# Optimization experiments

Measured on AMD Instinct MI355X. Metric: run time of the kernel, lower is better.

## Reference

```python
import jax, jax.numpy as jnp
import numpy as np

B, T, DMODEL = 2, 2048, 1024
H, DK, DV = 16, 64, 64
FF = 4096
EPS = 1e-5


def _layernorm_2d(x):
    # torch LayerNorm(normalized_shape=(T, dmodel)): normalize jointly over last two
    # dims, biased variance, weight=1 / bias=0 (freshly constructed each forward).
    mu = jnp.mean(x, axis=(1, 2), keepdims=True)
    var = jnp.mean((x - mu) ** 2, axis=(1, 2), keepdims=True)
    return (x - mu) / jnp.sqrt(var + EPS)


def setup_inputs() -> dict:
    key = jax.random.key(0)
    ks = jax.random.split(key, 9)
    s = 0.02  # small init for numerical sanity (original uses uniform(-1,1))
    return {
        "x": jax.random.normal(ks[0], (B, T, DMODEL), jnp.float32),
        "Wq": jax.random.normal(ks[1], (H, DMODEL, DK), jnp.float32) * s,
        "Wk": jax.random.normal(ks[2], (H, DMODEL, DK), jnp.float32) * s,
        "Wv": jax.random.normal(ks[3], (H, DMODEL, DV), jnp.float32) * s,
        "Wo": jax.random.normal(ks[4], (DMODEL, DMODEL), jnp.float32) * s,
        "W1": jax.random.normal(ks[5], (DMODEL, FF), jnp.float32) * s,
        "b1": jnp.zeros((FF,), jnp.float32),
        "W2": jax.random.normal(ks[6], (FF, DMODEL), jnp.float32) * s,
        "b2": jnp.zeros((DMODEL,), jnp.float32),
    }


def reference(x, Wq, Wk, Wv, Wo, W1, b1, W2, b2):
    b, t, d = x.shape
    h, _, dk = Wq.shape
    dv = Wv.shape[-1]
    # per-head projections: (B,H,T,dk/dv)
    Qp = jnp.einsum("btd,hdk->bhtk", x, Wq)
    Kp = jnp.einsum("btd,hdk->bhtk", x, Wk)
    Vp = jnp.einsum("btd,hdv->bhtv", x, Wv)
    scores = jnp.einsum("bhqk,bhsk->bhqs", Qp, Kp) / np.sqrt(dk).astype(np.float32)
    # NOTE: original does torch.softmax(heads, 2) -> softmax over the QUERY axis
    attn = jax.nn.softmax(scores, axis=2)
    heads = jnp.einsum("bhqs,bhsv->bqhv", attn, Vp).reshape(b, t, h * dv)
    att_out = heads @ Wo
    o1 = _layernorm_2d(x + att_out)
    ff = jnp.maximum(o1 @ W1 + b1, 0.0) @ W2 + b2
    return _layernorm_2d(o1 + ff)
```

## Files before the change

### kernel.cpp

```cpp
#include <hip/hip_runtime.h>
#include <hip/hip_bf16.h>
#include <cstddef>
#include <cstdint>

typedef __hip_bfloat16 hbf;
typedef __attribute__((ext_vector_type(8))) __bf16 bf16x8;
typedef __attribute__((ext_vector_type(4))) float f32x4;

#define B_ 2
#define T_ 2048
#define D_ 1024
#define H_ 16
#define FF_ 4096
#define EPS_ 1e-5f
#define SCALE_ 0.18033688011112f

__device__ __forceinline__ float bf2f(hbf v) { return __bfloat162float(v); }
__device__ __forceinline__ float fexp2(float x) {
  return __builtin_amdgcn_exp2f(x);
}
__device__ __forceinline__ float flog2(float x) {
  return __builtin_amdgcn_logf(x);
}
__device__ __forceinline__ float ldin(const void* p, size_t i, int isbf) {
  return isbf ? __bfloat162float(((const hbf*)p)[i]) : ((const float*)p)[i];
}
__device__ __forceinline__ void ston(void* p, size_t i, float v, int isbf) {
  if (isbf) ((hbf*)p)[i] = __float2bfloat16(v);
  else ((float*)p)[i] = v;
}
__device__ __forceinline__ f32x4 mfma16(bf16x8 a, bf16x8 b, f32x4 c) {
  return __builtin_amdgcn_mfma_f32_16x16x32_bf16(a, b, c, 0, 0, 0);
}
__device__ __forceinline__ bf16x8 ldfrag(const hbf* p) {
  return *(const bf16x8*)p;
}
__device__ __forceinline__ void glds16(const hbf* g, hbf* l) {
  __builtin_amdgcn_global_load_lds(
      (const __attribute__((address_space(1))) void*)g,
      (__attribute__((address_space(3))) void*)l, 16, 0, 0);
}

__global__ __launch_bounds__(256) void detect_dtype(const unsigned* x,
                                                    int* flag) {
  __shared__ int cnt[256];
  int c = 0;
  for (int i = threadIdx.x; i < 4096; i += 256) {
    unsigned low = x[i] & 0xFFFFu;
    unsigned e = (low >> 7) & 0xFFu;
    if (e >= 100u && e <= 142u) c++;
  }
  cnt[threadIdx.x] = c;
  __syncthreads();
  for (int off = 128; off > 0; off >>= 1) {
    if ((int)threadIdx.x < off) cnt[threadIdx.x] += cnt[threadIdx.x + off];
    __syncthreads();
  }
  if (threadIdx.x == 0) *flag = (cnt[0] > 2458) ? 1 : 0;
}

__device__ __forceinline__ void tr_tile(const void* __restrict__ src,
                                        hbf* __restrict__ dst, int R, int C,
                                        size_t zoff, int cx, int ry, int f,
                                        float (*tile)[33]) {
  const int tx = threadIdx.x & 31, ty = threadIdx.x >> 5;
  const int c0 = cx * 32, r0 = ry * 32;
#pragma unroll
  for (int p = 0; p < 4; p++) {
    int rr = p * 8 + ty;
    tile[rr][tx] = ldin(src, zoff + (size_t)(r0 + rr) * C + c0 + tx, f);
  }
  __syncthreads();
#pragma unroll
  for (int p = 0; p < 4; p++) {
    int cc = p * 8 + ty;
    dst[zoff + (size_t)(c0 + cc) * R + r0 + tx] = __float2bfloat16(tile[tx][cc]);
  }
}

__global__ __launch_bounds__(256) void preconv(
    const void* __restrict__ x, const void* __restrict__ Wq,
    const void* __restrict__ Wk, const void* __restrict__ Wv,
    const void* __restrict__ Wo, const void* __restrict__ W1,
    const void* __restrict__ W2, const void* __restrict__ b1,
    const void* __restrict__ b2, hbf* __restrict__ xb,
    hbf* __restrict__ wqkvt, hbf* __restrict__ wot, hbf* __restrict__ w1t,
    hbf* __restrict__ w2t, hbf* __restrict__ b1b, hbf* __restrict__ b2b,
    const int* __restrict__ flag) {
  __shared__ float tile[32][33];
  const int f = *flag;
  const int bid = blockIdx.x;
  if (bid < 3072) {
    int which = bid >> 10;
    int r = bid & 1023;
    int z = r >> 6, rem = r & 63;
    int ry = rem >> 1, cx = rem & 1;
    const void* src = (which == 0) ? Wq : (which == 1) ? Wk : Wv;
    hbf* dst = wqkvt + (size_t)which * (D_ * D_);
    tr_tile(src, dst, 1024, 64, (size_t)z * 65536, cx, ry, f, tile);
  } else if (bid < 4096) {
    int t = bid - 3072;
    tr_tile(Wo, wot, 1024, 1024, 0, t & 31, t >> 5, f, tile);
  } else if (bid < 8192) {
    int t = bid - 4096;
    tr_tile(W1, w1t, 1024, 4096, 0, t & 127, t >> 7, f, tile);
  } else if (bid < 12288) {
    int t = bid - 8192;
    tr_tile(W2, w2t, 4096, 1024, 0, t & 31, t >> 5, f, tile);
  } else if (bid < 13312) {
    size_t base = (size_t)(bid - 12288) * 4096;
    for (int i = threadIdx.x; i < 4096; i += 256)
      xb[base + i] = __float2bfloat16(ldin(x, base + i, f));
  } else if (bid == 13312) {
    for (int i = threadIdx.x; i < FF_; i += 256)
      b1b[i] = __float2bfloat16(ldin(b1, i, f));
  } else {
    for (int i = threadIdx.x; i < D_; i += 256)
      b2b[i] = __float2bfloat16(ldin(b2, i, f));
  }
}

template <int MODE, int BM, int BN>
__global__ __launch_bounds__(256) void gemm_bt(
    const hbf* __restrict__ A, const hbf* __restrict__ Bt, hbf* __restrict__ C,
    float* __restrict__ Cf0, float* __restrict__ Cf1,
    const hbf* __restrict__ e1, float* __restrict__ red, int M, int N, int K,
    int LDK) {
  constexpr int WM = BM / 2, WN = BN / 2;
  constexpr int IF = WM / 16, JF = WN / 16;
  __shared__ alignas(16) hbf As[BM * 64];
  __shared__ alignas(16) hbf Bs[BN * 64];
  const int tid = threadIdx.x;
  const int wave = tid >> 6, lane = tid & 63;
  const int quad = lane >> 4, l16 = lane & 15;
  const int m0 = blockIdx.y * BM, n0 = blockIdx.x * BN;
  const int mw = (wave >> 1) * WM, nw = (wave & 1) * WN;
  const int srow = tid >> 3;
  const int scol = (tid & 7) * 8;
  const int kbase = (MODE == 4) ? blockIdx.z * K : 0;
  const f32x4 zero = {0.f, 0.f, 0.f, 0.f};
  f32x4 acc[IF][JF];
#pragma unroll
  for (int i = 0; i < IF; i++)
#pragma unroll
    for (int j = 0; j < JF; j++) acc[i][j] = zero;

  const hbf* ga = &A[(size_t)(m0 + srow) * LDK + kbase + scol];
  const hbf* gb = &Bt[(size_t)(n0 + srow) * LDK + kbase + scol];
  hbf* lA = &As[wave * 512];
  hbf* lB = &Bs[wave * 512];

  for (int k0 = 0; k0 < K; k0 += 64) {
#pragma unroll
    for (int c = 0; c < BM / 32; c++)
      glds16(ga + (size_t)(c * 32) * LDK + k0, lA + c * 2048);
#pragma unroll
    for (int c = 0; c < BN / 32; c++)
      glds16(gb + (size_t)(c * 32) * LDK + k0, lB + c * 2048);
    __syncthreads();
    bf16x8 af[2][IF], bfr[2][JF];
#pragma unroll
    for (int h = 0; h < 2; h++) {
#pragma unroll
      for (int i = 0; i < IF; i++)
        af[h][i] = ldfrag(&As[(mw + i * 16 + l16) * 64 + h * 32 + quad * 8]);
#pragma unroll
      for (int j = 0; j < JF; j++)
        bfr[h][j] = ldfrag(&Bs[(nw + j * 16 + l16) * 64 + h * 32 + quad * 8]);
    }
#pragma unroll
    for (int h = 0; h < 2; h++)
#pragma unroll
      for (int i = 0; i < IF; i++)
#pragma unroll
        for (int j = 0; j < JF; j++)
          acc[i][j] = mfma16(af[h][i], bfr[h][j], acc[i][j]);
    __syncthreads();
  }
  float ssum = 0.f, ssq = 0.f;
#pragma unroll
  for (int i = 0; i < IF; i++)
#pragma unroll
    for (int j = 0; j < JF; j++)
#pragma unroll
      for (int r = 0; r < 4; r++) {
        int m = m0 + mw + i * 16 + quad * 4 + r;
        int n = n0 + nw + j * 16 + l16;
        float v = acc[i][j][r];
        if (MODE == 0) {
          int which = n >> 10, n1 = n & 1023;
          int h = n1 >> 6, cc = n1 & 63;
          int b = m >> 11, t = m & (T_ - 1);
          if (which == 0) v *= SCALE_;
          C[(size_t)which * ((size_t)B_ * H_ * T_ * 64) +
            (((size_t)(b * H_ + h)) * T_ + t) * 64 + cc] = __float2bfloat16(v);
        } else if (MODE == 1) {
          hbf hv = __float2bfloat16(v + bf2f(e1[(size_t)m * N + n]));
          C[(size_t)m * N + n] = hv;
          float fv = bf2f(hv);
          ssum += fv;
          ssq += fv * fv;
        } else if (MODE == 2) {
          C[(size_t)m * N + n] = __float2bfloat16(fmaxf(v + bf2f(e1[n]), 0.f));
        } else if (MODE == 4) {
          float* Cf = blockIdx.z ? Cf1 : Cf0;
          Cf[(size_t)m * N + n] = v;
        }
      }
  if (MODE == 1) {
    float* sc = (float*)As;
    sc[tid] = ssum;
    sc[256 + tid] = ssq;
    __syncthreads();
    for (int off = 128; off > 0; off >>= 1) {
      if (tid < off) {
        sc[tid] += sc[tid + off];
        sc[256 + tid] += sc[256 + tid + off];
      }
      __syncthreads();
    }
    if (tid == 0) {
      int b = m0 >> 11;
      atomicAdd(&red[b * 2 + 0], sc[0]);
      atomicAdd(&red[b * 2 + 1], sc[256]);
    }
  }
}

__global__ __launch_bounds__(256) void attn_stats(const hbf* __restrict__ Q,
                                                  const hbf* __restrict__ K,
                                                  const hbf* __restrict__ V,
                                                  hbf* __restrict__ Vt) {
  __shared__ alignas(16) hbf Ks[64 * 72];
  __shared__ alignas(16) hbf Qs[64 * 72];
  __shared__ float sAdj[64];
  const int bh = blockIdx.y;
  const int s0 = blockIdx.x * 64;
  const int tid = threadIdx.x;
  const int wave = tid >> 6, lane = tid & 63;
  const int quad = lane >> 4, l16 = lane & 15;
  const int sw = wave * 16;
  const hbf* Kb = K + (size_t)bh * T_ * 64;
  const hbf* Qb = Q + (size_t)bh * T_ * 64;
  const hbf* Vb = V + (size_t)bh * T_ * 64;
  hbf* Vtb = Vt + (size_t)bh * 64 * T_;
  const int r_ = tid >> 3, c_ = (tid & 7) * 8;
#pragma unroll
  for (int c = 0; c < 2; c++) {
    int row = c * 32 + r_;
    *(float4*)(&Ks[row * 72 + c_]) =
        *(const float4*)(&Kb[(size_t)(s0 + row) * 64 + c_]);
  }
  __syncthreads();
  bf16x8 kf0 = ldfrag(&Ks[(sw + l16) * 72 + quad * 8]);
  bf16x8 kf1 = ldfrag(&Ks[(sw + l16) * 72 + 32 + quad * 8]);
  float m_thr[4], l_thr[4];
#pragma unroll
  for (int r = 0; r < 4; r++) {
    m_thr[r] = -1e30f;
    l_thr[r] = 0.f;
  }
  const f32x4 zero = {0.f, 0.f, 0.f, 0.f};
  for (int qt = 0; qt < T_ / 64; qt++) {
    if (qt) __syncthreads();
#pragma unroll
    for (int c = 0; c < 2; c++) {
      int row = c * 32 + r_;
      *(float4*)(&Qs[row * 72 + c_]) =
          *(const float4*)(&Qb[(size_t)(qt * 64 + row) * 64 + c_]);
    }
    __syncthreads();
    f32x4 acc[4];
#pragma unroll
    for (int j = 0; j < 4; j++) {
      bf16x8 qf0 = ldfrag(&Qs[(j * 16 + l16) * 72 + quad * 8]);
      bf16x8 qf1 = ldfrag(&Qs[(j * 16 + l16) * 72 + 32 + quad * 8]);
      f32x4 a = zero;
      a = mfma16(kf0, qf0, a);
      a = mfma16(kf1, qf1, a);
      acc[j] = a;
    }
#pragma unroll
    for (int r = 0; r < 4; r++) {
      float mt = fmaxf(fmaxf(acc[0][r], acc[1][r]),
                       fmaxf(acc[2][r], acc[3][r]));
      float nm = fmaxf(m_thr[r], mt);
      float s = l_thr[r] * fexp2(m_thr[r] - nm);
#pragma unroll
      for (int j = 0; j < 4; j++) s += fexp2(acc[j][r] - nm);
      l_thr[r] = s;
      m_thr[r] = nm;
    }
  }
#pragma unroll
  for (int d = 1; d < 16; d <<= 1) {
#pragma unroll
    for (int r = 0; r < 4; r++) {
      float om = __shfl_xor(m_thr[r], d);
      float ol = __shfl_xor(l_thr[r], d);
      float nm = fmaxf(m_thr[r], om);
      l_thr[r] = l_thr[r] * fexp2(m_thr[r] - nm) + ol * fexp2(om - nm);
      m_thr[r] = nm;
    }
  }
  if (l16 == 0) {
#pragma unroll
    for (int r = 0; r < 4; r++)
      sAdj[sw + quad * 4 + r] = m_thr[r] + flog2(l_thr[r]);
  }
  __syncthreads();
#pragma unroll
  for (int c = 0; c < 2; c++) {
    int e = (c * 256 + tid) * 8;
    int r = e >> 6, col = e & 63;
    union alignas(16) {
      hbf h[8];
      float4 f4;
    } u;
    u.f4 = *(const float4*)(&Vb[(size_t)(s0 + r) * 64 + col]);
    float sc = fexp2(-sAdj[r]);
#pragma unroll
    for (int k2 = 0; k2 < 8; k2++)
      u.h[k2] = __float2bfloat16(bf2f(u.h[k2]) * sc);
    *(float4*)(&Ks[r * 72 + col]) = u.f4;
  }
  __syncthreads();
#pragma unroll
  for (int c = 0; c < 2; c++) {
    int e = (c * 256 + tid) * 8;
    int v = e >> 6, tt = e & 63;
    union alignas(16) {
      hbf h[8];
      float4 f4;
    } u;
#pragma unroll
    for (int k2 = 0; k2 < 8; k2++) u.h[k2] = Ks[(tt + k2) * 72 + v];
    *(float4*)(&Vtb[(size_t)v * T_ + s0 + tt]) = u.f4;
  }
}

__global__ __launch_bounds__(256) void attn_apply(const hbf* __restrict__ Q,
                                                  const hbf* __restrict__ K,
                                                  const hbf* __restrict__ Vt,
                                                  hbf* __restrict__ heads) {
  __shared__ alignas(16) hbf Ksb[2 * 64 * 64];
  __shared__ alignas(16) hbf Vsb[2 * 64 * 64];
  __shared__ alignas(16) hbf Ps[4 * 32 * 72];
  const int bh = blockIdx.y;
  const int b = bh >> 4, h = bh & 15;
  const int q0 = blockIdx.x * 128;
  const int tid = threadIdx.x;
  const int wave = tid >> 6, lane = tid & 63;
  const int quad = lane >> 4, l16 = lane & 15;
  const int qw = wave * 32;
  const hbf* Qb = Q + (size_t)bh * T_ * 64;
  const hbf* Kb = K + (size_t)bh * T_ * 64;
  const hbf* Vtb = Vt + (size_t)bh * 64 * T_;
  hbf* Pw = &Ps[wave * 32 * 72];
  const int srow = tid >> 3, sc8 = tid & 7;
  const int swz = sc8 ^ (srow & 7);
  const hbf* gk = Kb + (size_t)srow * 64 + swz * 8;
  const hbf* gv = Vtb + (size_t)srow * T_ + swz * 8;
  hbf* lK = &Ksb[wave * 512];
  hbf* lV = &Vsb[wave * 512];
  const int sx = (l16 & 7) * 8;
  bf16x8 qf[2][2];
#pragma unroll
  for (int i = 0; i < 2; i++)
#pragma unroll
    for (int hh = 0; hh < 2; hh++)
      qf[i][hh] = ldfrag(&Qb[(size_t)(q0 + qw + i * 16 + l16) * 64 + hh * 32 +
                             quad * 8]);
  const f32x4 zero = {0.f, 0.f, 0.f, 0.f};
  f32x4 accO[2][4];
#pragma unroll
  for (int i = 0; i < 2; i++)
#pragma unroll
    for (int j = 0; j < 4; j++) accO[i][j] = zero;

  glds16(gk, lK);
  glds16(gk + 2048, lK + 2048);
  glds16(gv, lV);
  glds16(gv + (size_t)32 * T_, lV + 2048);
  __syncthreads();

  for (int st = 0; st < T_ / 64; st++) {
    const int cur = st & 1, nxt = cur ^ 1;
    if (st < T_ / 64 - 1) {
      size_t ko = (size_t)(st + 1) * 4096;
      glds16(gk + ko, lK + nxt * 4096);
      glds16(gk + ko + 2048, lK + nxt * 4096 + 2048);
      glds16(gv + (st + 1) * 64, lV + nxt * 4096);
      glds16(gv + (size_t)32 * T_ + (st + 1) * 64, lV + nxt * 4096 + 2048);
    }
    const hbf* Kc = &Ksb[cur * 4096];
    const hbf* Vc = &Vsb[cur * 4096];
    bf16x8 kf[4][2];
#pragma unroll
    for (int j = 0; j < 4; j++)
#pragma unroll
      for (int hh = 0; hh < 2; hh++)
        kf[j][hh] =
            ldfrag(&Kc[(j * 16 + l16) * 64 + ((hh * 32 + quad * 8) ^ sx)]);
    f32x4 accS[2][4];
#pragma unroll
    for (int i = 0; i < 2; i++)
#pragma unroll
      for (int j = 0; j < 4; j++) {
        f32x4 a = mfma16(kf[j][0], qf[i][0], zero);
        accS[i][j] = mfma16(kf[j][1], qf[i][1], a);
      }
#pragma unroll
    for (int i = 0; i < 2; i++)
#pragma unroll
      for (int j = 0; j < 4; j++) {
        union {
          hbf h4[4];
          uint2 u;
        } pk;
#pragma unroll
        for (int r = 0; r < 4; r++)
          pk.h4[r] = __float2bfloat16(fexp2(accS[i][j][r]));
        *(uint2*)&Pw[(i * 16 + l16) * 72 + j * 16 + quad * 4] = pk.u;
      }
    bf16x8 pf[2][2];
#pragma unroll
    for (int i = 0; i < 2; i++)
#pragma unroll
      for (int hh = 0; hh < 2; hh++)
        pf[i][hh] = ldfrag(&Pw[(i * 16 + l16) * 72 + hh * 32 + quad * 8]);
#pragma unroll
    for (int j2 = 0; j2 < 4; j2++) {
      bf16x8 vf0 = ldfrag(&Vc[(j2 * 16 + l16) * 64 + ((quad * 8) ^ sx)]);
      bf16x8 vf1 = ldfrag(&Vc[(j2 * 16 + l16) * 64 + ((32 + quad * 8) ^ sx)]);
#pragma unroll
      for (int i = 0; i < 2; i++) {
        accO[i][j2] = mfma16(pf[i][0], vf0, accO[i][j2]);
        accO[i][j2] = mfma16(pf[i][1], vf1, accO[i][j2]);
      }
    }
    __syncthreads();
  }
#pragma unroll
  for (int i = 0; i < 2; i++)
#pragma unroll
    for (int j2 = 0; j2 < 4; j2++)
#pragma unroll
      for (int r = 0; r < 4; r++) {
        int q = q0 + qw + i * 16 + quad * 4 + r;
        int v = j2 * 16 + l16;
        heads[((size_t)(b * T_ + q)) * D_ + h * 64 + v] =
            __float2bfloat16(accO[i][j2][r]);
      }
}

__global__ __launch_bounds__(256) void ln_norm(const hbf* __restrict__ src,
                                               const float* __restrict__ red,
                                               void* dst,
                                               const int* __restrict__ flag,
                                               int force_bf) {
  const int isbf = force_bf ? 1 : *flag;
  const float invN = 1.f / (float)(T_ * D_);
  for (size_t i = (size_t)blockIdx.x * 256 + threadIdx.x;
       i < (size_t)B_ * T_ * D_; i += (size_t)gridDim.x * 256) {
    int b = (int)(i >> 21);
    float mu = red[b * 2 + 0] * invN;
    float var = red[b * 2 + 1] * invN - mu * mu;
    ston(dst, i, (bf2f(src[i]) - mu) * rsqrtf(var + EPS_), isbf);
  }
}

__global__ __launch_bounds__(256) void ln2_stats(const float* __restrict__ P0,
                                                 const float* __restrict__ P1,
                                                 const hbf* __restrict__ o1,
                                                 const hbf* __restrict__ b2b,
                                                 float* __restrict__ red) {
  __shared__ float s1[256], s2[256];
  const int b = blockIdx.y;
  const size_t base = (size_t)b * (T_ * D_);
  float sum = 0.f, sq = 0.f;
  for (size_t i = (size_t)blockIdx.x * 256 + threadIdx.x; i < (size_t)T_ * D_;
       i += (size_t)gridDim.x * 256) {
    size_t e = base + i;
    float v = P0[e] + P1[e] + bf2f(b2b[i & (D_ - 1)]) + bf2f(o1[e]);
    sum += v;
    sq += v * v;
  }
  s1[threadIdx.x] = sum;
  s2[threadIdx.x] = sq;
  __syncthreads();
  for (int off = 128; off > 0; off >>= 1) {
    if ((int)threadIdx.x < off) {
      s1[threadIdx.x] += s1[threadIdx.x + off];
      s2[threadIdx.x] += s2[threadIdx.x + off];
    }
    __syncthreads();
  }
  if (threadIdx.x == 0) {
    atomicAdd(&red[b * 2 + 0], s1[0]);
    atomicAdd(&red[b * 2 + 1], s2[0]);
  }
}

__global__ __launch_bounds__(256) void ln2_norm(
    const float* __restrict__ P0, const float* __restrict__ P1,
    const hbf* __restrict__ o1, const hbf* __restrict__ b2b,
    const float* __restrict__ red, void* dst, const int* __restrict__ flag) {
  const int isbf = *flag;
  const float invN = 1.f / (float)(T_ * D_);
  for (size_t i = (size_t)blockIdx.x * 256 + threadIdx.x;
       i < (size_t)B_ * T_ * D_; i += (size_t)gridDim.x * 256) {
    int b = (int)(i >> 21);
    float mu = red[b * 2 + 0] * invN;
    float var = red[b * 2 + 1] * invN - mu * mu;
    float v = P0[i] + P1[i] + bf2f(b2b[i & (D_ - 1)]) + bf2f(o1[i]);
    ston(dst, i, (v - mu) * rsqrtf(var + EPS_), isbf);
  }
}

extern "C" void kernel_launch(void* const* d_in, const int* in_sizes, int n_in,
                              void* d_out, int out_size, void* d_ws,
                              size_t ws_size, hipStream_t stream) {
  const void* x = d_in[0];
  const void* Wq = d_in[1];
  const void* Wk = d_in[2];
  const void* Wv = d_in[3];
  const void* Wo = d_in[4];
  const void* W1 = d_in[5];
  const void* W2 = d_in[7];
  const void* b1 = d_in[6];
  const void* b2 = d_in[8];

  const size_t MB = 1024 * 1024;
  if (ws_size < 89 * MB) return;

  char* w = (char*)d_ws;
  hbf* xb = (hbf*)(w + 0 * MB);
  hbf* wqkvt = (hbf*)(w + 8 * MB);
  hbf* wot = (hbf*)(w + 14 * MB);
  hbf* w1t = (hbf*)(w + 16 * MB);
  hbf* w2t = (hbf*)(w + 24 * MB);
  hbf* Qb = (hbf*)(w + 32 * MB);
  hbf* Kb = (hbf*)(w + 40 * MB);
  hbf* Vb = (hbf*)(w + 48 * MB);
  hbf* Vtb = (hbf*)(w + 56 * MB);
  hbf* heads = (hbf*)(w + 64 * MB);
  hbf* r1 = (hbf*)(w + 72 * MB);
  hbf* o1 = (hbf*)(w + 80 * MB);
  hbf* ff1 = (hbf*)(w + 32 * MB);
  float* P0 = (float*)(w + 0 * MB);
  float* P1 = (float*)(w + 64 * MB);
  hbf* b1b = (hbf*)(w + 88 * MB);
  hbf* b2b = b1b + FF_;
  float* red = (float*)(b2b + D_);
  int* flag = (int*)(red + 8);

  hipMemsetAsync(red, 0, 8 * sizeof(float) + sizeof(int), stream);
  detect_dtype<<<1, 256, 0, stream>>>((const unsigned*)x, flag);

  const int M = B_ * T_;
  preconv<<<13314, 256, 0, stream>>>(x, Wq, Wk, Wv, Wo, W1, W2, b1, b2, xb,
                                     wqkvt, wot, w1t, w2t, b1b, b2b, flag);
  gemm_bt<0, 128, 128><<<dim3(24, 32), 256, 0, stream>>>(
      xb, wqkvt, Qb, nullptr, nullptr, nullptr, nullptr, M, 3 * D_, D_, D_);
  attn_stats<<<dim3(32, 32), 256, 0, stream>>>(Qb, Kb, Vb, Vtb);
  attn_apply<<<dim3(16, 32), 256, 0, stream>>>(Qb, Kb, Vtb, heads);
  gemm_bt<1, 128, 64><<<dim3(16, 32), 256, 0, stream>>>(
      heads, wot, r1, nullptr, nullptr, xb, red, M, D_, D_, D_);
  ln_norm<<<4096, 256, 0, stream>>>(r1, red, o1, flag, 1);
  gemm_bt<2, 128, 128><<<dim3(32, 32), 256, 0, stream>>>(
      o1, w1t, ff1, nullptr, nullptr, b1b, nullptr, M, FF_, D_, D_);
  gemm_bt<4, 128, 128><<<dim3(8, 32, 2), 256, 0, stream>>>(
      ff1, w2t, nullptr, P0, P1, nullptr, nullptr, M, D_, FF_ / 2, FF_);
  ln2_stats<<<dim3(256, B_), 256, 0, stream>>>(P0, P1, o1, b2b, red + 4);
  ln2_norm<<<2048, 256, 0, stream>>>(P0, P1, o1, b2b, red + 4, d_out, flag);
}
```

Baseline: 461.8 us.

## Software-pipeline attention apply across tiles and vectorize input conversion

The attention-apply loop is restructured so each iteration does the P·V product for the previous tile while computing QK scores and exp for the current one. To support this it adds a third V buffer and a second P buffer per wave in LDS, plus a prologue and epilogue. The aim is to overlap MFMA work with the exp/convert work and hide LDS latency, with s_setprio raising wave priority around the MFMA blocks. Separately, the x-to-bf16 conversion now uses 16-byte vector loads and stores; the cost is more LDS per block, which may lower occupancy.

```diff
diff --git a/kernel.cpp b/kernel.cpp
--- a/kernel.cpp
+++ b/kernel.cpp
@@ -109,8 +109,29 @@
     tr_tile(W2, w2t, 4096, 1024, 0, t & 31, t >> 5, f, tile);
   } else if (bid < 13312) {
     size_t base = (size_t)(bid - 12288) * 4096;
-    for (int i = threadIdx.x; i < 4096; i += 256)
-      xb[base + i] = __float2bfloat16(ldin(x, base + i, f));
+    if (f) {
+      const uint4* src = (const uint4*)((const hbf*)x + base);
+      uint4* dst = (uint4*)(xb + base);
+      for (int i = threadIdx.x; i < 512; i += 256) dst[i] = src[i];
+    } else {
+      const float4* src = (const float4*)((const float*)x + base);
+      for (int i = threadIdx.x; i < 512; i += 256) {
+        float4 a = src[i * 2], b = src[i * 2 + 1];
+        union {
+          hbf h[8];
+          uint4 u;
+        } o;
+        o.h[0] = __float2bfloat16(a.x);
+        o.h[1] = __float2bfloat16(a.y);
+        o.h[2] = __float2bfloat16(a.z);
+        o.h[3] = __float2bfloat16(a.w);
+        o.h[4] = __float2bfloat16(b.x);
+        o.h[5] = __float2bfloat16(b.y);
+        o.h[6] = __float2bfloat16(b.z);
+        o.h[7] = __float2bfloat16(b.w);
+        *(uint4*)(xb + base + (size_t)i * 8) = o.u;
+      }
+    }
   } else if (bid == 13312) {
     for (int i = threadIdx.x; i < FF_; i += 256)
       b1b[i] = __float2bfloat16(ldin(b1, i, f));
@@ -344,8 +365,8 @@
                                                   const hbf* __restrict__ Vt,
                                                   hbf* __restrict__ heads) {
   __shared__ alignas(16) hbf Ksb[2 * 64 * 64];
-  __shared__ alignas(16) hbf Vsb[2 * 64 * 64];
-  __shared__ alignas(16) hbf Ps[4 * 32 * 72];
+  __shared__ alignas(16) hbf Vsb[3 * 64 * 64];
+  __shared__ alignas(16) hbf Ps[4 * 2 * 32 * 72];
   const int bh = blockIdx.y;
   const int b = bh >> 4, h = bh & 15;
   const int q0 = blockIdx.x * 128;
@@ -356,7 +377,7 @@
   const hbf* Qb = Q + (size_t)bh * T_ * 64;
   const hbf* Kb = K + (size_t)bh * T_ * 64;
   const hbf* Vtb = Vt + (size_t)bh * 64 * T_;
-  hbf* Pw = &Ps[wave * 32 * 72];
+  hbf* Pw = &Ps[wave * (2 * 32 * 72)];
   const int srow = tid >> 3, sc8 = tid & 7;
   const int swz = sc8 ^ (srow & 7);
   const hbf* gk = Kb + (size_t)srow * 64 + swz * 8;
@@ -382,19 +403,14 @@
   glds16(gk + 2048, lK + 2048);
   glds16(gv, lV);
   glds16(gv + (size_t)32 * T_, lV + 2048);
-  __syncthreads();
-
-  for (int st = 0; st < T_ / 64; st++) {
-    const int cur = st & 1, nxt = cur ^ 1;
-    if (st < T_ / 64 - 1) {
-      size_t ko = (size_t)(st + 1) * 4096;
-      glds16(gk + ko, lK + nxt * 4096);
-      glds16(gk + ko + 2048, lK + nxt * 4096 + 2048);
-      glds16(gv + (st + 1) * 64, lV + nxt * 4096);
-      glds16(gv + (size_t)32 * T_ + (st + 1) * 64, lV + nxt * 4096 + 2048);
-    }
-    const hbf* Kc = &Ksb[cur * 4096];
-    const hbf* Vc = &Vsb[cur * 4096];
+  glds16(gk + 4096, lK + 4096);
+  glds16(gk + 4096 + 2048, lK + 4096 + 2048);
+  glds16(gv + 64, lV + 4096);
+  glds16(gv + (size_t)32 * T_ + 64, lV + 4096 + 2048);
+  __syncthreads();
+
+  {
+    const hbf* Kc = &Ksb[0];
     bf16x8 kf[4][2];
 #pragma unroll
     for (int j = 0; j < 4; j++)
@@ -402,6 +418,7 @@
       for (int hh = 0; hh < 2; hh++)
         kf[j][hh] =
             ldfrag(&Kc[(j * 16 + l16) * 64 + ((hh * 32 + quad * 8) ^ sx)]);
+    __builtin_amdgcn_s_setprio(1);
     f32x4 accS[2][4];
 #pragma unroll
     for (int i = 0; i < 2; i++)
@@ -410,6 +427,7 @@
         f32x4 a = mfma16(kf[j][0], qf[i][0], zero);
         accS[i][j] = mfma16(kf[j][1], qf[i][1], a);
       }
+    __builtin_amdgcn_s_setprio(0);
 #pragma unroll
     for (int i = 0; i < 2; i++)
 #pragma unroll
@@ -423,23 +441,95 @@
           pk.h4[r] = __float2bfloat16(fexp2(accS[i][j][r]));
         *(uint2*)&Pw[(i * 16 + l16) * 72 + j * 16 + quad * 4] = pk.u;
       }
+  }
+  __syncthreads();
+
+  for (int st = 1; st < T_ / 64; st++) {
+    const int kcur = st & 1;
+    const int pcur = st & 1, pprev = pcur ^ 1;
+    const int vprev = (st - 1) % 3;
+    if (st < T_ / 64 - 1) {
+      const int knxt = (st + 1) & 1, vnxt = (st + 1) % 3;
+      size_t ko = (size_t)(st + 1) * 4096;
+      glds16(gk + ko, lK + knxt * 4096);
+      glds16(gk + ko + 2048, lK + knxt * 4096 + 2048);
+      glds16(gv + (st + 1) * 64, lV + vnxt * 4096);
+      glds16(gv + (size_t)32 * T_ + (st + 1) * 64, lV + vnxt * 4096 + 2048);
+    }
+    const hbf* Kc = &Ksb[kcur * 4096];
+    const hbf* Vp = &Vsb[vprev * 4096];
+    bf16x8 kf[4][2];
+#pragma unroll
+    for (int j = 0; j < 4; j++)
+#pragma unroll
+      for (int hh = 0; hh < 2; hh++)
+        kf[j][hh] =
+            ldfrag(&Kc[(j * 16 + l16) * 64 + ((hh * 32 + quad * 8) ^ sx)]);
     bf16x8 pf[2][2];
 #pragma unroll
     for (int i = 0; i < 2; i++)
 #pragma unroll
       for (int hh = 0; hh < 2; hh++)
-        pf[i][hh] = ldfrag(&Pw[(i * 16 + l16) * 72 + hh * 32 + quad * 8]);
+        pf[i][hh] = ldfrag(
+            &Pw[pprev * (32 * 72) + (i * 16 + l16) * 72 + hh * 32 + quad * 8]);
+    __builtin_amdgcn_s_setprio(1);
 #pragma unroll
     for (int j2 = 0; j2 < 4; j2++) {
-      bf16x8 vf0 = ldfrag(&Vc[(j2 * 16 + l16) * 64 + ((quad * 8) ^ sx)]);
-      bf16x8 vf1 = ldfrag(&Vc[(j2 * 16 + l16) * 64 + ((32 + quad * 8) ^ sx)]);
+      bf16x8 vf0 = ldfrag(&Vp[(j2 * 16 + l16) * 64 + ((quad * 8) ^ sx)]);
+      bf16x8 vf1 = ldfrag(&Vp[(j2 * 16 + l16) * 64 + ((32 + quad * 8) ^ sx)]);
 #pragma unroll
       for (int i = 0; i < 2; i++) {
         accO[i][j2] = mfma16(pf[i][0], vf0, accO[i][j2]);
         accO[i][j2] = mfma16(pf[i][1], vf1, accO[i][j2]);
       }
     }
+    f32x4 accS[2][4];
+#pragma unroll
+    for (int i = 0; i < 2; i++)
+#pragma unroll
+      for (int j = 0; j < 4; j++) {
+        f32x4 a = mfma16(kf[j][0], qf[i][0], zero);
+        accS[i][j] = mfma16(kf[j][1], qf[i][1], a);
+      }
+    __builtin_amdgcn_s_setprio(0);
+#pragma unroll
+    for (int i = 0; i < 2; i++)
+#pragma unroll
+      for (int j = 0; j < 4; j++) {
+        union {
+          hbf h4[4];
+          uint2 u;
+        } pk;
+#pragma unroll
+        for (int r = 0; r < 4; r++)
+          pk.h4[r] = __float2bfloat16(fexp2(accS[i][j][r]));
+        *(uint2*)&Pw[pcur * (32 * 72) + (i * 16 + l16) * 72 + j * 16 +
+                     quad * 4] = pk.u;
+      }
     __syncthreads();
+  }
+  {
+    const int pl = (T_ / 64 - 1) & 1;
+    const hbf* Vp = &Vsb[((T_ / 64 - 1) % 3) * 4096];
+    bf16x8 pf[2][2];
+#pragma unroll
+    for (int i = 0; i < 2; i++)
+#pragma unroll
+      for (int hh = 0; hh < 2; hh++)
+        pf[i][hh] = ldfrag(
+            &Pw[pl * (32 * 72) + (i * 16 + l16) * 72 + hh * 32 + quad * 8]);
+    __builtin_amdgcn_s_setprio(1);
+#pragma unroll
+    for (int j2 = 0; j2 < 4; j2++) {
+      bf16x8 vf0 = ldfrag(&Vp[(j2 * 16 + l16) * 64 + ((quad * 8) ^ sx)]);
+      bf16x8 vf1 = ldfrag(&Vp[(j2 * 16 + l16) * 64 + ((32 + quad * 8) ^ sx)]);
+#pragma unroll
+      for (int i = 0; i < 2; i++) {
+        accO[i][j2] = mfma16(pf[i][0], vf0, accO[i][j2]);
+        accO[i][j2] = mfma16(pf[i][1], vf1, accO[i][j2]);
+      }
+    }
+    __builtin_amdgcn_s_setprio(0);
   }
 #pragma unroll
   for (int i = 0; i < 2; i++)
```

New measurement: 452.5 us. 2.0% less time.
